# Performance work log

Hardware: AMD Instinct MI355X
Metric: run time of the kernel (lower is better)

Reference implementation:

```python
import jax, jax.numpy as jnp
import numpy as np

KCODES = 8  # kcodes from init


def setup_inputs() -> dict:
    key = jax.random.key(0)
    k1, k2 = jax.random.split(key)
    x = jax.random.normal(k1, (4, 2048, 768), dtype=jnp.float32)          # [B, S, D]
    codebook = jax.random.normal(k2, (8192, 768), dtype=jnp.float32)      # [N, D] embedding weight
    return {"x": x, "codebook": codebook}


def reference(x, codebook):
    # EuclideanSnapFunction.forward with default hook_kwargs
    # (keep_k_codes=True, no disabled codes/tokens):
    #   logits = -cdist(x, codebook, p=2); topk(kcodes); gather; mean over k.
    # Top-k over -dist is identical to top-k over -dist^2, so we use squared
    x2 = jnp.sum(x * x, axis=-1, keepdims=True)                 # [B, S, 1]
    c2 = jnp.sum(codebook * codebook, axis=-1)                  # [N]
    xc = jnp.einsum('bsd,nd->bsn', x, codebook)                 # [B, S, N]
    neg_d2 = 2.0 * xc - x2 - c2                                 # -squared dist
    _, codebook_ids = jax.lax.top_k(neg_d2, KCODES)             # [B, S, K]
    quant = codebook[codebook_ids]                              # [B, S, K, D] gather
    outputs = quant.sum(axis=-2) / KCODES                       # masked averaging over k codes
    return outputs, codebook_ids
```

## Files before the change

### kernel.cpp

```cpp
#include <hip/hip_runtime.h>

#define T_TOK 8192
#define DIM   768
#define NCB   8192
#define KSEL  8
#define BT    64
#define BN    128
#define BD    32
#define NQ    (BD/4)
#define DSTR  140
#define BUFQ  1536

typedef float v2f __attribute__((ext_vector_type(2)));

__device__ __forceinline__ void gload16(const float* g, float4* l) {
  __builtin_amdgcn_global_load_lds(
      (const __attribute__((address_space(1))) void*)g,
      (__attribute__((address_space(3))) void*)l, 16, 0, 0);
}

__global__ __launch_bounds__(256) void sq_pairwise_kernel(
    const float* __restrict__ cb, const float* __restrict__ x,
    float* __restrict__ c2out, float* __restrict__ x2out)
{
  #pragma clang fp contract(off)
  __shared__ float part[32][8];
  const int tid = threadIdx.x;
  const int row = blockIdx.x * 32 + (tid >> 3);
  const int b   = tid & 7;
  const float* src = (row < NCB) ? (cb + (size_t)row * DIM)
                                 : (x + (size_t)(row - NCB) * DIM);
  const float* a = src + 96 * b;

  float s[16];
  #pragma unroll
  for (int l = 0; l < 16; ++l) {
    float v, t;
    v = a[l];       t = v * v; float r0 = t;
    v = a[64 + l];  t = v * v; r0 = r0 + t;
    v = a[80 + l];  t = v * v; r0 = r0 + t;
    v = a[16 + l];  t = v * v; float r1 = t;
    v = a[32 + l];  t = v * v; float r2 = t;
    v = a[48 + l];  t = v * v; float r3 = t;
    s[l] = (r0 + r1) + (r2 + r3);
  }
  float t1[8], t2[4];
  #pragma unroll
  for (int i = 0; i < 8; ++i) t1[i] = s[i] + s[i + 8];
  #pragma unroll
  for (int j = 0; j < 4; ++j) t2[j] = t1[j] + t1[j + 4];
  part[tid >> 3][b] = (t2[0] + t2[2]) + (t2[1] + t2[3]);
  __syncthreads();

  if (b == 0) {
    const float* p = part[tid >> 3];
    float res = ((p[0] + p[1]) + (p[2] + p[3])) + ((p[4] + p[5]) + (p[6] + p[7]));
    if (row < NCB) c2out[row] = res;
    else           x2out[row - NCB] = res;
  }
}

__global__ __launch_bounds__(256, 2) void dist_topk_kernel(
    const float* __restrict__ x, const float* __restrict__ cb,
    const float* __restrict__ c2g, const float* __restrict__ x2g,
    float* __restrict__ ws, int ncodes)
{
  #pragma clang fp contract(off)
  __shared__ float4 smem4[2 * BUFQ];
  float* smem = (float*)smem4;

  const int tid  = threadIdx.x;
  const int t0   = blockIdx.x * BT;
  const int nbeg = blockIdx.y * ncodes;

  const int gx = tid & 15;
  const int gy = tid >> 4;
  const int g7 = gx & 7;

  const int tt = tid >> 2;
  const int cc = tid & 3;

  const int lane = tid & 63;
  const int wid  = tid >> 6;

  const float* xsrcA = x + (size_t)(t0 + lane) * DIM + wid * 4;
  const float* xsrcB = xsrcA + 16;

  const int s0_ = 0 * 256 + wid * 64 + lane;
  const int s1_ = 1 * 256 + wid * 64 + lane;
  const int s2_ = 2 * 256 + wid * 64 + lane;
  const int s3_ = 3 * 256 + wid * 64 + lane;
  const int c0_ = s0_ >> 3, q0_ = (s0_ & 7) ^ ((s0_ >> 6) & 7);
  const int c1_ = s1_ >> 3, q1_ = (s1_ & 7) ^ ((s1_ >> 6) & 7);
  const int c2_ = s2_ >> 3, q2_ = (s2_ & 7) ^ ((s2_ >> 6) & 7);
  const int c3_ = s3_ >> 3, q3_ = (s3_ & 7) ^ ((s3_ >> 6) & 7);

  float x2r[4];
  #pragma unroll
  for (int i = 0; i < 4; ++i) x2r[i] = x2g[t0 + gy * 4 + i];

  float bdist[KSEL]; int bid[KSEL];
  #pragma unroll
  for (int i = 0; i < KSEL; ++i) { bdist[i] = __builtin_inff(); bid[i] = 0x7fffffff; }
  float bmax = __builtin_inff(); int bmaxid = 0x7fffffff; int bslot = 0;

  for (int n0 = nbeg; n0 < nbeg + ncodes; n0 += BN) {
    float c2r[8];
    #pragma unroll
    for (int j = 0; j < 8; ++j) c2r[j] = c2g[n0 + gx * 8 + j];

    v2f accL[4][8], accH[4][8];
    #pragma unroll
    for (int i = 0; i < 4; ++i)
      #pragma unroll
      for (int j = 0; j < 8; ++j) { accL[i][j] = (v2f)0.f; accH[i][j] = (v2f)0.f; }

    const float* csrc0 = cb + (size_t)(n0 + c0_) * DIM + q0_ * 4;
    const float* csrc1 = cb + (size_t)(n0 + c1_) * DIM + q1_ * 4;
    const float* csrc2 = cb + (size_t)(n0 + c2_) * DIM + q2_ * 4;
    const float* csrc3 = cb + (size_t)(n0 + c3_) * DIM + q3_ * 4;

    __syncthreads();
    {
      float4* xsn = smem4;
      float4* csn = smem4 + 512;
      gload16(xsrcA, xsn + wid * 64);
      gload16(xsrcB, xsn + 256 + wid * 64);
      gload16(csrc0, csn + 0   + wid * 64);
      gload16(csrc1, csn + 256 + wid * 64);
      gload16(csrc2, csn + 512 + wid * 64);
      gload16(csrc3, csn + 768 + wid * 64);
    }
    __syncthreads();

    for (int d0 = 0; d0 < DIM; d0 += BD) {
      const int buf = (d0 >> 5) & 1;
      const float4* xsb = smem4 + buf * BUFQ;
      const float4* csb = xsb + 512;

      const int dn = d0 + BD;
      if (dn < DIM) {
        float4* xsn = smem4 + (buf ^ 1) * BUFQ;
        float4* csn = xsn + 512;
        gload16(xsrcA + dn, xsn + wid * 64);
        gload16(xsrcB + dn, xsn + 256 + wid * 64);
        gload16(csrc0 + dn, csn + 0   + wid * 64);
        gload16(csrc1 + dn, csn + 256 + wid * 64);
        gload16(csrc2 + dn, csn + 512 + wid * 64);
        gload16(csrc3 + dn, csn + 768 + wid * 64);
      }

      #pragma unroll
      for (int q = 0; q < NQ; ++q) {
        float4 xa[4];
        #pragma unroll
        for (int i = 0; i < 4; ++i) xa[i] = xsb[q * BT + gy * 4 + i];
        const float4* cq = csb + gx * 64 + (q ^ g7);
        #pragma unroll
        for (int j = 0; j < 8; ++j) {
          const float4 cv = cq[j * 8];
          #pragma unroll
          for (int i = 0; i < 4; ++i) {
            v2f a, b, p;
            a[0] = xa[i].x; a[1] = xa[i].y;
            b[0] = cv.x;    b[1] = cv.y;
            p = a * b;
            accL[i][j] = accL[i][j] + p;
            a[0] = xa[i].z; a[1] = xa[i].w;
            b[0] = cv.z;    b[1] = cv.w;
            p = a * b;
            accH[i][j] = accH[i][j] + p;
          }
        }
      }
      __syncthreads();
    }

    #pragma unroll
    for (int i = 0; i < 4; ++i) {
      float v[8];
      #pragma unroll
      for (int j = 0; j < 8; ++j) {
        float xc = (accL[i][j][0] + accH[i][j][0]) + (accL[i][j][1] + accH[i][j][1]);
        float s  = 2.0f * xc - x2r[i];
        v[j] = -(s - c2r[j]);
      }
      float4* dp = (float4*)&smem[(gy * 4 + i) * DSTR + gx * 8];
      dp[0] = make_float4(v[0], v[1], v[2], v[3]);
      dp[1] = make_float4(v[4], v[5], v[6], v[7]);
    }
    __syncthreads();

    #pragma unroll
    for (int i2 = 0; i2 < BN / 4; ++i2) {
      const float dval = smem[tt * DSTR + cc + 4 * i2];
      const int   id   = n0 + cc + 4 * i2;
      if (dval < bmax) {
        #pragma unroll
        for (int q = 0; q < KSEL; ++q)
          if (q == bslot) { bdist[q] = dval; bid[q] = id; }
        bmax = bdist[0]; bmaxid = bid[0]; bslot = 0;
        #pragma unroll
        for (int q = 1; q < KSEL; ++q)
          if (bdist[q] > bmax || (bdist[q] == bmax && bid[q] > bmaxid)) {
            bmax = bdist[q]; bmaxid = bid[q]; bslot = q;
          }
      }
    }
  }

  __syncthreads();
  float* md = smem;
  int*   mi = (int*)smem + 2048;
  #pragma unroll
  for (int j = 0; j < KSEL; ++j) {
    md[tt * 32 + cc * KSEL + j] = bdist[j];
    mi[tt * 32 + cc * KSEL + j] = bid[j];
  }
  __syncthreads();
  if (tid < BT) {
    float* mdt = md + tid * 32;
    int*   mit = mi + tid * 32;
    const size_t base = ((size_t)blockIdx.y * T_TOK + (t0 + tid)) * 16;
    for (int r = 0; r < KSEL; ++r) {
      float best = __builtin_inff(); int bestid = 0x7fffffff; int bs = 0;
      for (int s = 0; s < 32; ++s) {
        const float dv = mdt[s]; const int iv = mit[s];
        if (dv < best || (dv == best && iv < bestid)) { best = dv; bestid = iv; bs = s; }
      }
      mdt[bs] = __builtin_inff();
      ws[base + r] = best;
      ((int*)ws)[base + 8 + r] = bestid;
    }
  }
}

__global__ __launch_bounds__(192) void merge_gather_kernel(
    const float* __restrict__ cb, const float* __restrict__ ws,
    float* __restrict__ out, float* __restrict__ out_ids, int nsplit)
{
  __shared__ float mv[64];
  __shared__ int   mid[64];
  __shared__ int   ssel[KSEL];

  const int t   = blockIdx.x;
  const int tid = threadIdx.x;
  const int ncand = nsplit * KSEL;

  if (tid < ncand) {
    const int s = tid >> 3, r = tid & 7;
    const size_t base = ((size_t)s * T_TOK + t) * 16;
    mv[tid]  = ws[base + r];
    mid[tid] = ((const int*)ws)[base + 8 + r];
  }
  __syncthreads();

  if (tid == 0) {
    for (int r = 0; r < KSEL; ++r) {
      float best = __builtin_inff(); int bestid = 0x7fffffff; int bs = 0;
      for (int s = 0; s < ncand; ++s) {
        const float dv = mv[s]; const int iv = mid[s];
        if (dv < best || (dv == best && iv < bestid)) { best = dv; bestid = iv; bs = s; }
      }
      mv[bs] = __builtin_inff();
      ssel[r] = bestid;
      out_ids[(size_t)t * KSEL + r] = (float)bestid;
    }
  }
  __syncthreads();

  float4 s4 = make_float4(0.f, 0.f, 0.f, 0.f);
  #pragma unroll
  for (int r = 0; r < KSEL; ++r) {
    const float4 v = *(const float4*)(cb + (size_t)ssel[r] * DIM + tid * 4);
    s4.x += v.x; s4.y += v.y; s4.z += v.z; s4.w += v.w;
  }
  s4.x *= 0.125f; s4.y *= 0.125f; s4.z *= 0.125f; s4.w *= 0.125f;
  *(float4*)(out + (size_t)t * DIM + tid * 4) = s4;
}

extern "C" void kernel_launch(void* const* d_in, const int* in_sizes, int n_in,
                              void* d_out, int out_size, void* d_ws, size_t ws_size,
                              hipStream_t stream) {
  (void)in_sizes; (void)n_in; (void)out_size;
  const float* x   = (const float*)d_in[0];
  const float* cbk = (const float*)d_in[1];
  float* out     = (float*)d_out;
  float* c2buf   = out;
  float* x2buf   = out + NCB;
  float* out_ids = out + (size_t)T_TOK * DIM;
  float* ws      = (float*)d_ws;

  int nsplit = 1;
  for (int s = 4; s >= 1; s >>= 1) {
    if ((size_t)s * T_TOK * 16 * 4 <= ws_size) { nsplit = s; break; }
  }
  const int ncodes = NCB / nsplit;

  sq_pairwise_kernel<<<(NCB + T_TOK) / 32, 256, 0, stream>>>(cbk, x, c2buf, x2buf);
  dist_topk_kernel<<<dim3(T_TOK / BT, nsplit), 256, 0, stream>>>(
      x, cbk, c2buf, x2buf, ws, ncodes);
  merge_gather_kernel<<<T_TOK, 192, 0, stream>>>(cbk, ws, out, out_ids, nsplit);
}
```

Before: 2.430 ms.

## Halve token tile and split the depth reduction across two thread halves

The token tile per block shrinks from 64 to 32, and the 256 threads split into two halves. Each half accumulates a different pair of lanes within each float4 of the depth dimension, so the accumulator array per thread is halved. The partial sums are combined through shared memory in two passes before the distance write, the top-k scan uses 8 threads per token, and launch bounds move from 2 to 4 blocks to target higher occupancy. In exchange the kernel adds extra synchronisations and shared-memory exchange traffic, loads the codebook twice as often per token, and the final merge scans 64 candidates per token instead of 32.

```diff
diff --git a/kernel.cpp b/kernel.cpp
--- a/kernel.cpp
+++ b/kernel.cpp
@@ -4,12 +4,13 @@
 #define DIM   768
 #define NCB   8192
 #define KSEL  8
-#define BT    64
+#define BT    32
 #define BN    128
 #define BD    32
-#define NQ    (BD/4)
 #define DSTR  140
-#define BUFQ  1536
+#define BUFQ  1280
+#define EXOFF 4608
+#define MSTR  66
 
 typedef float v2f __attribute__((ext_vector_type(2)));
 
@@ -60,7 +61,7 @@
   }
 }
 
-__global__ __launch_bounds__(256, 2) void dist_topk_kernel(
+__global__ __launch_bounds__(256, 4) void dist_topk_kernel(
     const float* __restrict__ x, const float* __restrict__ cb,
     const float* __restrict__ c2g, const float* __restrict__ x2g,
     float* __restrict__ ws, int ncodes)
@@ -73,27 +74,27 @@
   const int t0   = blockIdx.x * BT;
   const int nbeg = blockIdx.y * ncodes;
 
-  const int gx = tid & 15;
-  const int gy = tid >> 4;
-  const int g7 = gx & 7;
-
-  const int tt = tid >> 2;
-  const int cc = tid & 3;
-
-  const int lane = tid & 63;
-  const int wid  = tid >> 6;
-
-  const float* xsrcA = x + (size_t)(t0 + lane) * DIM + wid * 4;
-  const float* xsrcB = xsrcA + 16;
-
-  const int s0_ = 0 * 256 + wid * 64 + lane;
-  const int s1_ = 1 * 256 + wid * 64 + lane;
-  const int s2_ = 2 * 256 + wid * 64 + lane;
-  const int s3_ = 3 * 256 + wid * 64 + lane;
-  const int c0_ = s0_ >> 3, q0_ = (s0_ & 7) ^ ((s0_ >> 6) & 7);
-  const int c1_ = s1_ >> 3, q1_ = (s1_ & 7) ^ ((s1_ >> 6) & 7);
-  const int c2_ = s2_ >> 3, q2_ = (s2_ & 7) ^ ((s2_ >> 6) & 7);
-  const int c3_ = s3_ >> 3, q3_ = (s3_ & 7) ^ ((s3_ >> 6) & 7);
+  const int pid = tid & 127;
+  const int h   = tid >> 7;
+  const int gx  = pid & 15;
+  const int gy  = pid >> 4;
+  const int g7  = gx & 7;
+
+  const int tt = tid >> 3;
+  const int cc = tid & 7;
+
+  const int wb = tid & ~63;
+
+  const float* xsrc = x + (size_t)(t0 + (tid & 31)) * DIM + (tid >> 5) * 4;
+
+  int coff[4];
+  #pragma unroll
+  for (int m = 0; m < 4; ++m) {
+    const int s = m * 256 + tid;
+    const int c = s >> 3;
+    const int q = (s & 7) ^ ((s >> 6) & 7);
+    coff[m] = c * DIM + q * 4;
+  }
 
   float x2r[4];
   #pragma unroll
@@ -105,96 +106,93 @@
   float bmax = __builtin_inff(); int bmaxid = 0x7fffffff; int bslot = 0;
 
   for (int n0 = nbeg; n0 < nbeg + ncodes; n0 += BN) {
-    float c2r[8];
-    #pragma unroll
-    for (int j = 0; j < 8; ++j) c2r[j] = c2g[n0 + gx * 8 + j];
-
-    v2f accL[4][8], accH[4][8];
+    const float* cbn = cb + (size_t)n0 * DIM;
+
+    v2f acc[4][8];
     #pragma unroll
     for (int i = 0; i < 4; ++i)
       #pragma unroll
-      for (int j = 0; j < 8; ++j) { accL[i][j] = (v2f)0.f; accH[i][j] = (v2f)0.f; }
-
-    const float* csrc0 = cb + (size_t)(n0 + c0_) * DIM + q0_ * 4;
-    const float* csrc1 = cb + (size_t)(n0 + c1_) * DIM + q1_ * 4;
-    const float* csrc2 = cb + (size_t)(n0 + c2_) * DIM + q2_ * 4;
-    const float* csrc3 = cb + (size_t)(n0 + c3_) * DIM + q3_ * 4;
+      for (int j = 0; j < 8; ++j) acc[i][j] = (v2f)0.f;
 
     __syncthreads();
     {
-      float4* xsn = smem4;
-      float4* csn = smem4 + 512;
-      gload16(xsrcA, xsn + wid * 64);
-      gload16(xsrcB, xsn + 256 + wid * 64);
-      gload16(csrc0, csn + 0   + wid * 64);
-      gload16(csrc1, csn + 256 + wid * 64);
-      gload16(csrc2, csn + 512 + wid * 64);
-      gload16(csrc3, csn + 768 + wid * 64);
+      gload16(xsrc, smem4 + wb);
+      #pragma unroll
+      for (int m = 0; m < 4; ++m)
+        gload16(cbn + coff[m], smem4 + 256 + m * 256 + wb);
     }
     __syncthreads();
 
     for (int d0 = 0; d0 < DIM; d0 += BD) {
       const int buf = (d0 >> 5) & 1;
-      const float4* xsb = smem4 + buf * BUFQ;
-      const float4* csb = xsb + 512;
-
       const int dn = d0 + BD;
       if (dn < DIM) {
-        float4* xsn = smem4 + (buf ^ 1) * BUFQ;
-        float4* csn = xsn + 512;
-        gload16(xsrcA + dn, xsn + wid * 64);
-        gload16(xsrcB + dn, xsn + 256 + wid * 64);
-        gload16(csrc0 + dn, csn + 0   + wid * 64);
-        gload16(csrc1 + dn, csn + 256 + wid * 64);
-        gload16(csrc2 + dn, csn + 512 + wid * 64);
-        gload16(csrc3 + dn, csn + 768 + wid * 64);
-      }
-
+        float4* nb = smem4 + (buf ^ 1) * BUFQ;
+        gload16(xsrc + dn, nb + wb);
+        #pragma unroll
+        for (int m = 0; m < 4; ++m)
+          gload16(cbn + coff[m] + dn, nb + 256 + m * 256 + wb);
+      }
+
+      const char* xb  = (const char*)(smem4 + buf * BUFQ) + gy * 64 + h * 8;
+      const char* cb8 = (const char*)(smem4 + buf * BUFQ + 256) + gx * 1024 + h * 8;
       #pragma unroll
-      for (int q = 0; q < NQ; ++q) {
-        float4 xa[4];
-        #pragma unroll
-        for (int i = 0; i < 4; ++i) xa[i] = xsb[q * BT + gy * 4 + i];
-        const float4* cq = csb + gx * 64 + (q ^ g7);
+      for (int q = 0; q < 8; ++q) {
+        const v2f xa0 = *(const v2f*)(xb + q * 512);
+        const v2f xa1 = *(const v2f*)(xb + q * 512 + 16);
+        const v2f xa2 = *(const v2f*)(xb + q * 512 + 32);
+        const v2f xa3 = *(const v2f*)(xb + q * 512 + 48);
+        const char* cq = cb8 + ((q ^ g7) << 4);
         #pragma unroll
         for (int j = 0; j < 8; ++j) {
-          const float4 cv = cq[j * 8];
+          const v2f cv = *(const v2f*)(cq + j * 128);
+          v2f p;
+          p = xa0 * cv; acc[0][j] = acc[0][j] + p;
+          p = xa1 * cv; acc[1][j] = acc[1][j] + p;
+          p = xa2 * cv; acc[2][j] = acc[2][j] + p;
+          p = xa3 * cv; acc[3][j] = acc[3][j] + p;
+        }
+      }
+      __syncthreads();
+    }
+
+    #pragma unroll
+    for (int jb = 0; jb < 8; jb += 4) {
+      if (h) {
+        float* ex = smem + EXOFF + pid * 34;
+        #pragma unroll
+        for (int i = 0; i < 4; ++i)
           #pragma unroll
-          for (int i = 0; i < 4; ++i) {
-            v2f a, b, p;
-            a[0] = xa[i].x; a[1] = xa[i].y;
-            b[0] = cv.x;    b[1] = cv.y;
-            p = a * b;
-            accL[i][j] = accL[i][j] + p;
-            a[0] = xa[i].z; a[1] = xa[i].w;
-            b[0] = cv.z;    b[1] = cv.w;
-            p = a * b;
-            accH[i][j] = accH[i][j] + p;
+          for (int j2 = 0; j2 < 4; ++j2)
+            *(v2f*)(ex + (i * 4 + j2) * 2) = acc[i][jb + j2];
+      }
+      __syncthreads();
+      if (!h) {
+        float c2r[4];
+        #pragma unroll
+        for (int j2 = 0; j2 < 4; ++j2) c2r[j2] = c2g[n0 + gx * 8 + jb + j2];
+        const float* ex = smem + EXOFF + pid * 34;
+        #pragma unroll
+        for (int i = 0; i < 4; ++i) {
+          float v[4];
+          #pragma unroll
+          for (int j2 = 0; j2 < 4; ++j2) {
+            const v2f b = *(const v2f*)(ex + (i * 4 + j2) * 2);
+            const float xc = (acc[i][jb + j2][0] + b[0]) + (acc[i][jb + j2][1] + b[1]);
+            const float s  = 2.0f * xc - x2r[i];
+            v[j2] = -(s - c2r[j2]);
           }
+          *(float4*)&smem[(gy * 4 + i) * DSTR + gx * 8 + jb] =
+              make_float4(v[0], v[1], v[2], v[3]);
         }
       }
       __syncthreads();
     }
 
     #pragma unroll
-    for (int i = 0; i < 4; ++i) {
-      float v[8];
-      #pragma unroll
-      for (int j = 0; j < 8; ++j) {
-        float xc = (accL[i][j][0] + accH[i][j][0]) + (accL[i][j][1] + accH[i][j][1]);
-        float s  = 2.0f * xc - x2r[i];
-        v[j] = -(s - c2r[j]);
-      }
-      float4* dp = (float4*)&smem[(gy * 4 + i) * DSTR + gx * 8];
-      dp[0] = make_float4(v[0], v[1], v[2], v[3]);
-      dp[1] = make_float4(v[4], v[5], v[6], v[7]);
-    }
-    __syncthreads();
-
-    #pragma unroll
-    for (int i2 = 0; i2 < BN / 4; ++i2) {
-      const float dval = smem[tt * DSTR + cc + 4 * i2];
-      const int   id   = n0 + cc + 4 * i2;
+    for (int i2 = 0; i2 < BN / 8; ++i2) {
+      const float dval = smem[tt * DSTR + cc + 8 * i2];
+      const int   id   = n0 + cc + 8 * i2;
       if (dval < bmax) {
         #pragma unroll
         for (int q = 0; q < KSEL; ++q)
@@ -211,20 +209,20 @@
 
   __syncthreads();
   float* md = smem;
-  int*   mi = (int*)smem + 2048;
+  int*   mi = (int*)smem + 32 * MSTR;
   #pragma unroll
   for (int j = 0; j < KSEL; ++j) {
-    md[tt * 32 + cc * KSEL + j] = bdist[j];
-    mi[tt * 32 + cc * KSEL + j] = bid[j];
+    md[tt * MSTR + cc * KSEL + j] = bdist[j];
+    mi[tt * MSTR + cc * KSEL + j] = bid[j];
   }
   __syncthreads();
   if (tid < BT) {
-    float* mdt = md + tid * 32;
-    int*   mit = mi + tid * 32;
+    float* mdt = md + tid * MSTR;
+    int*   mit = mi + tid * MSTR;
     const size_t base = ((size_t)blockIdx.y * T_TOK + (t0 + tid)) * 16;
     for (int r = 0; r < KSEL; ++r) {
       float best = __builtin_inff(); int bestid = 0x7fffffff; int bs = 0;
-      for (int s = 0; s < 32; ++s) {
+      for (int s = 0; s < 64; ++s) {
         const float dv = mdt[s]; const int iv = mit[s];
         if (dv < best || (dv == best && iv < bestid)) { best = dv; bestid = iv; bs = s; }
       }
```

New measurement: 2.842 ms. 1.17x slower.

## Shrink dist tile to 32 codes with per-thread token ownership and inline top-k

Applied to the files above, without the earlier changes.

Replaces the 64x128 register-blocked tile (4x8 outputs per thread, top-k run from a shared-memory distance staging pass) with a 64x32 tile. Each thread now owns one token and 8 codes and feeds its distances straight into its private top-k, with no staging pass. This drops a shared-memory round trip and a barrier per tile, halves LDS so occupancy can rise to 4 blocks per CU, and raises the code-split count to 8. The cost is far less register reuse: each x load now feeds only 8 codes instead of 32, so the compute-to-LDS-load ratio falls sharply and the x tile is re-streamed for every 32 codes.

```diff
diff --git a/kernel.cpp b/kernel.cpp
--- a/kernel.cpp
+++ b/kernel.cpp
@@ -5,11 +5,10 @@
 #define NCB   8192
 #define KSEL  8
 #define BT    64
-#define BN    128
+#define CTILE 32
 #define BD    32
-#define NQ    (BD/4)
-#define DSTR  140
-#define BUFQ  1536
+#define BUFQ  768
+#define MST   33
 
 typedef float v2f __attribute__((ext_vector_type(2)));
 
@@ -60,7 +59,7 @@
   }
 }
 
-__global__ __launch_bounds__(256, 2) void dist_topk_kernel(
+__global__ __launch_bounds__(256, 4) void dist_topk_kernel(
     const float* __restrict__ x, const float* __restrict__ cb,
     const float* __restrict__ c2g, const float* __restrict__ x2g,
     float* __restrict__ ws, int ncodes)
@@ -72,129 +71,72 @@
   const int tid  = threadIdx.x;
   const int t0   = blockIdx.x * BT;
   const int nbeg = blockIdx.y * ncodes;
-
-  const int gx = tid & 15;
-  const int gy = tid >> 4;
-  const int g7 = gx & 7;
-
-  const int tt = tid >> 2;
-  const int cc = tid & 3;
-
   const int lane = tid & 63;
-  const int wid  = tid >> 6;
-
-  const float* xsrcA = x + (size_t)(t0 + lane) * DIM + wid * 4;
-  const float* xsrcB = xsrcA + 16;
-
-  const int s0_ = 0 * 256 + wid * 64 + lane;
-  const int s1_ = 1 * 256 + wid * 64 + lane;
-  const int s2_ = 2 * 256 + wid * 64 + lane;
-  const int s3_ = 3 * 256 + wid * 64 + lane;
-  const int c0_ = s0_ >> 3, q0_ = (s0_ & 7) ^ ((s0_ >> 6) & 7);
-  const int c1_ = s1_ >> 3, q1_ = (s1_ & 7) ^ ((s1_ >> 6) & 7);
-  const int c2_ = s2_ >> 3, q2_ = (s2_ & 7) ^ ((s2_ >> 6) & 7);
-  const int c3_ = s3_ >> 3, q3_ = (s3_ & 7) ^ ((s3_ >> 6) & 7);
-
-  float x2r[4];
-  #pragma unroll
-  for (int i = 0; i < 4; ++i) x2r[i] = x2g[t0 + gy * 4 + i];
+  const int w    = tid >> 6;
+
+  const float* xrow = x + (size_t)(t0 + lane) * DIM;
+  const float* crow = cb + (size_t)(tid >> 3) * DIM + (tid & 7) * 4;
+  float4* xdst = smem4 + (tid & ~63);
+  float4* cdst = smem4 + 512 + (tid & ~63);
+
+  const float x2r = x2g[t0 + lane];
 
   float bdist[KSEL]; int bid[KSEL];
   #pragma unroll
   for (int i = 0; i < KSEL; ++i) { bdist[i] = __builtin_inff(); bid[i] = 0x7fffffff; }
   float bmax = __builtin_inff(); int bmaxid = 0x7fffffff; int bslot = 0;
 
-  for (int n0 = nbeg; n0 < nbeg + ncodes; n0 += BN) {
-    float c2r[8];
+  for (int n0 = nbeg; n0 < nbeg + ncodes; n0 += CTILE) {
+    v2f accL[8], accH[8];
     #pragma unroll
-    for (int j = 0; j < 8; ++j) c2r[j] = c2g[n0 + gx * 8 + j];
-
-    v2f accL[4][8], accH[4][8];
-    #pragma unroll
-    for (int i = 0; i < 4; ++i)
-      #pragma unroll
-      for (int j = 0; j < 8; ++j) { accL[i][j] = (v2f)0.f; accH[i][j] = (v2f)0.f; }
-
-    const float* csrc0 = cb + (size_t)(n0 + c0_) * DIM + q0_ * 4;
-    const float* csrc1 = cb + (size_t)(n0 + c1_) * DIM + q1_ * 4;
-    const float* csrc2 = cb + (size_t)(n0 + c2_) * DIM + q2_ * 4;
-    const float* csrc3 = cb + (size_t)(n0 + c3_) * DIM + q3_ * 4;
-
-    __syncthreads();
+    for (int j = 0; j < 8; ++j) { accL[j] = (v2f)0.f; accH[j] = (v2f)0.f; }
+
+    const size_t cb_tile = (size_t)n0 * DIM;
     {
-      float4* xsn = smem4;
-      float4* csn = smem4 + 512;
-      gload16(xsrcA, xsn + wid * 64);
-      gload16(xsrcB, xsn + 256 + wid * 64);
-      gload16(csrc0, csn + 0   + wid * 64);
-      gload16(csrc1, csn + 256 + wid * 64);
-      gload16(csrc2, csn + 512 + wid * 64);
-      gload16(csrc3, csn + 768 + wid * 64);
+      gload16(xrow + w * 4,      xdst);
+      gload16(xrow + 16 + w * 4, xdst + 256);
+      gload16(crow + cb_tile,    cdst);
     }
     __syncthreads();
 
     for (int d0 = 0; d0 < DIM; d0 += BD) {
       const int buf = (d0 >> 5) & 1;
-      const float4* xsb = smem4 + buf * BUFQ;
-      const float4* csb = xsb + 512;
-
       const int dn = d0 + BD;
       if (dn < DIM) {
-        float4* xsn = smem4 + (buf ^ 1) * BUFQ;
-        float4* csn = xsn + 512;
-        gload16(xsrcA + dn, xsn + wid * 64);
-        gload16(xsrcB + dn, xsn + 256 + wid * 64);
-        gload16(csrc0 + dn, csn + 0   + wid * 64);
-        gload16(csrc1 + dn, csn + 256 + wid * 64);
-        gload16(csrc2 + dn, csn + 512 + wid * 64);
-        gload16(csrc3 + dn, csn + 768 + wid * 64);
-      }
-
+        float4* xd = xdst + (buf ^ 1) * BUFQ;
+        gload16(xrow + dn + w * 4,      xd);
+        gload16(xrow + dn + 16 + w * 4, xd + 256);
+        gload16(crow + cb_tile + dn,    cdst + (buf ^ 1) * BUFQ);
+      }
+
+      const char* xb  = (const char*)(smem4 + buf * BUFQ) + lane * 16;
+      const char* cbp = (const char*)(smem4 + buf * BUFQ + 512) + w * 1024;
       #pragma unroll
-      for (int q = 0; q < NQ; ++q) {
-        float4 xa[4];
-        #pragma unroll
-        for (int i = 0; i < 4; ++i) xa[i] = xsb[q * BT + gy * 4 + i];
-        const float4* cq = csb + gx * 64 + (q ^ g7);
+      for (int q = 0; q < 8; ++q) {
+        const float4 xv = *(const float4*)(xb + q * 1024);
+        v2f xlo, xhi;
+        xlo[0] = xv.x; xlo[1] = xv.y;
+        xhi[0] = xv.z; xhi[1] = xv.w;
         #pragma unroll
         for (int j = 0; j < 8; ++j) {
-          const float4 cv = cq[j * 8];
-          #pragma unroll
-          for (int i = 0; i < 4; ++i) {
-            v2f a, b, p;
-            a[0] = xa[i].x; a[1] = xa[i].y;
-            b[0] = cv.x;    b[1] = cv.y;
-            p = a * b;
-            accL[i][j] = accL[i][j] + p;
-            a[0] = xa[i].z; a[1] = xa[i].w;
-            b[0] = cv.z;    b[1] = cv.w;
-            p = a * b;
-            accH[i][j] = accH[i][j] + p;
-          }
+          const float4 cv = *(const float4*)(cbp + j * 128 + q * 16);
+          v2f clo, chi, p;
+          clo[0] = cv.x; clo[1] = cv.y;
+          chi[0] = cv.z; chi[1] = cv.w;
+          p = xlo * clo; accL[j] = accL[j] + p;
+          p = xhi * chi; accH[j] = accH[j] + p;
         }
       }
       __syncthreads();
     }
 
     #pragma unroll
-    for (int i = 0; i < 4; ++i) {
-      float v[8];
-      #pragma unroll
-      for (int j = 0; j < 8; ++j) {
-        float xc = (accL[i][j][0] + accH[i][j][0]) + (accL[i][j][1] + accH[i][j][1]);
-        float s  = 2.0f * xc - x2r[i];
-        v[j] = -(s - c2r[j]);
-      }
-      float4* dp = (float4*)&smem[(gy * 4 + i) * DSTR + gx * 8];
-      dp[0] = make_float4(v[0], v[1], v[2], v[3]);
-      dp[1] = make_float4(v[4], v[5], v[6], v[7]);
-    }
-    __syncthreads();
-
-    #pragma unroll
-    for (int i2 = 0; i2 < BN / 4; ++i2) {
-      const float dval = smem[tt * DSTR + cc + 4 * i2];
-      const int   id   = n0 + cc + 4 * i2;
+    for (int j = 0; j < 8; ++j) {
+      const float c2 = c2g[n0 + w * 8 + j];
+      const float xc = (accL[j][0] + accH[j][0]) + (accL[j][1] + accH[j][1]);
+      const float s  = 2.0f * xc - x2r;
+      const float dval = -(s - c2);
+      const int   id   = n0 + w * 8 + j;
       if (dval < bmax) {
         #pragma unroll
         for (int q = 0; q < KSEL; ++q)
@@ -209,18 +151,17 @@
     }
   }
 
-  __syncthreads();
   float* md = smem;
-  int*   mi = (int*)smem + 2048;
+  int*   mi = (int*)smem + 64 * MST;
   #pragma unroll
   for (int j = 0; j < KSEL; ++j) {
-    md[tt * 32 + cc * KSEL + j] = bdist[j];
-    mi[tt * 32 + cc * KSEL + j] = bid[j];
+    md[lane * MST + w * KSEL + j] = bdist[j];
+    mi[lane * MST + w * KSEL + j] = bid[j];
   }
   __syncthreads();
   if (tid < BT) {
-    float* mdt = md + tid * 32;
-    int*   mit = mi + tid * 32;
+    float* mdt = md + tid * MST;
+    int*   mit = mi + tid * MST;
     const size_t base = ((size_t)blockIdx.y * T_TOK + (t0 + tid)) * 16;
     for (int r = 0; r < KSEL; ++r) {
       float best = __builtin_inff(); int bestid = 0x7fffffff; int bs = 0;
@@ -292,7 +233,7 @@
   float* ws      = (float*)d_ws;
 
   int nsplit = 1;
-  for (int s = 4; s >= 1; s >>= 1) {
+  for (int s = 8; s >= 1; s >>= 1) {
     if ((size_t)s * T_TOK * 16 * 4 <= ws_size) { nsplit = s; break; }
   }
   const int ncodes = NCB / nsplit;
```

Result: slower. 2.949 ms (+21.4%).
